# Kernel tuning notes

Hardware: AMD Instinct MI355X
Metric: run time of the kernel (lower is better)

The kernel has to match this reference:

```python
import jax, jax.numpy as jnp
import numpy as np

N_HEAD = 8
TOTAL_DIM = 64   # trans dim: num_node*f_dim + arV_dim = 15*4 + 4
F_DIM = 4        # node_feature_dim
NUM_NODE = 15
EPS = 1e-5


def _ln(x, g, b):
    m = jnp.mean(x, axis=-1, keepdims=True)
    v = jnp.var(x, axis=-1, keepdims=True)
    return (x - m) * jax.lax.rsqrt(v + EPS) * g + b


def setup_inputs() -> dict:
    key = jax.random.key(0)
    B, T, C, L, V = 4, 1024, 1024, 4, 100
    ks = jax.random.split(key, 16)
    g = lambda k, sh, s=0.02: jax.random.normal(k, sh, jnp.float32) * s
    return {
        'x': jax.random.normal(ks[0], (B, T, C), jnp.float32),
        'attn_bias': jax.random.normal(ks[1], (N_HEAD, NUM_NODE, NUM_NODE), jnp.float32),
        'pos_emb': g(ks[2], (1, T, C)),
        'Wq': g(ks[3], (L, C, C)), 'bq': jnp.zeros((L, C), jnp.float32),
        'Wk': g(ks[4], (L, C, C)), 'bk': jnp.zeros((L, C), jnp.float32),
        'Wv': g(ks[5], (L, C, C)), 'bv': jnp.zeros((L, C), jnp.float32),
        'Wp': g(ks[6], (L, C, C)), 'bp': jnp.zeros((L, C), jnp.float32),
        'ln1_g': jnp.ones((L, C), jnp.float32), 'ln1_b': jnp.zeros((L, C), jnp.float32),
        'ln2_g': jnp.ones((L, C), jnp.float32), 'ln2_b': jnp.zeros((L, C), jnp.float32),
        'w1': g(ks[7], (L, C, 4 * C)), 'b1': jnp.zeros((L, 4 * C), jnp.float32),
        'w2': g(ks[8], (L, 4 * C, C)), 'b2': jnp.zeros((L, C), jnp.float32),
        'lnf_g': jnp.ones((C,), jnp.float32), 'lnf_b': jnp.zeros((C,), jnp.float32),
        'head_w': g(ks[9], (TOTAL_DIM, V + 1, C)),
    }


def reference(x, attn_bias, pos_emb, Wq, bq, Wk, bk, Wv, bv, Wp, bp,
              ln1_g, ln1_b, ln2_g, ln2_b, w1, b1, w2, b2, lnf_g, lnf_b, head_w):
    B, T, C = x.shape
    L = Wq.shape[0]
    hd = C // N_HEAD
    scale = 1.0 / np.sqrt(hd).astype(np.float32)

    # expand graph bias: bias[h, i*f+a, j*f+b] = attn_bias[h, i, j]
    d = NUM_NODE * F_DIM
    bias = jnp.repeat(jnp.repeat(attn_bias, F_DIM, axis=1), F_DIM, axis=2)  # [nh, d, d]
    pbias = jnp.zeros((N_HEAD, T, T), x.dtype).at[:, :d, :d].set(bias)      # [nh, T, T]

    # causal mask with every TOTAL_DIM-th column disabled
    mask = jnp.tril(jnp.ones((T, T), bool))
    mask = mask & ((jnp.arange(T) % TOTAL_DIM) != TOTAL_DIM - 1)[None, :]

    h = x + pos_emb[:, :T]
    neg_inf = jnp.asarray(-jnp.inf, x.dtype)
    for l in range(L):  # fixed small layer count
        a = _ln(h, ln1_g[l], ln1_b[l])
        q = (a @ Wq[l] + bq[l]).reshape(B, T, N_HEAD, hd).transpose(0, 2, 1, 3)
        k = (a @ Wk[l] + bk[l]).reshape(B, T, N_HEAD, hd).transpose(0, 2, 1, 3)
        v = (a @ Wv[l] + bv[l]).reshape(B, T, N_HEAD, hd).transpose(0, 2, 1, 3)
        att = jnp.einsum('bhid,bhjd->bhij', q, k) * scale + pbias[None]
        att = jnp.where(mask[None, None], att, neg_inf)
        att = jax.nn.softmax(att, axis=-1)
        y = jnp.einsum('bhij,bhjd->bhid', att, v).transpose(0, 2, 1, 3).reshape(B, T, C)
        h = h + y @ Wp[l] + bp[l]
        a2 = _ln(h, ln2_g[l], ln2_b[l])
        h = h + jax.nn.gelu(a2 @ w1[l] + b1[l], approximate=False) @ w2[l] + b2[l]

    h = _ln(h, lnf_g, lnf_b)
    # pad_to_full_observation + EinLinear head
    n_pad = (-T) % TOTAL_DIM
    hp = jnp.pad(h, ((0, 0), (0, n_pad), (0, 0))).reshape(-1, TOTAL_DIM, C)
    logits = jnp.einsum('eoi,bei->beo', head_w, hp)
    return logits.reshape(B, T + n_pad, -1)[:, :T]
```

## Files before the change

### kernel.cpp

```cpp
#include <hip/hip_runtime.h>
#include <cstdint>

#define DEV __device__ __forceinline__

typedef unsigned short u16;
typedef __attribute__((ext_vector_type(8))) short bf16x8;
typedef __attribute__((ext_vector_type(4))) unsigned short u16x4;
typedef __attribute__((ext_vector_type(4))) float f32x4;

typedef __attribute__((address_space(1))) const void GV;
typedef __attribute__((address_space(3))) void LV;

DEV float b2f(u16 u) { uint32_t i = ((uint32_t)u) << 16; return __builtin_bit_cast(float, i); }
DEV u16 f2b(float f) {
    uint32_t i = __builtin_bit_cast(uint32_t, f);
    return (u16)((i + 0x7fffu + ((i >> 16) & 1u)) >> 16);
}
DEV void load_lds16(const void* g, void* l) {
    __builtin_amdgcn_global_load_lds((GV*)g, (LV*)l, 16, 0, 0);
}

__global__ __launch_bounds__(256) void k_addpos(const float* __restrict__ x,
                                                const float* __restrict__ pos,
                                                float* __restrict__ h) {
    size_t i = (size_t)blockIdx.x * 256 + threadIdx.x;
    f32x4 a = *(const f32x4*)(x + i * 4);
    f32x4 p = *(const f32x4*)(pos + ((i * 4) & 1048575));
    a += p;
    *(f32x4*)(h + i * 4) = a;
}

__global__ __launch_bounds__(256) void k_transcvt(const float* __restrict__ W,
                                                  u16* __restrict__ WT, int K, int N,
                                                  size_t ozs) {
    __shared__ float t[32][33];
    size_t zin = (size_t)blockIdx.z * K * N, zout = (size_t)blockIdx.z * ozs;
    int n0 = blockIdx.x * 32, k0 = blockIdx.y * 32;
    int r = threadIdx.x >> 3, c = (threadIdx.x & 7) << 2;
    f32x4 v = *(const f32x4*)(W + zin + (size_t)(k0 + r) * N + n0 + c);
    t[r][c] = v[0]; t[r][c + 1] = v[1]; t[r][c + 2] = v[2]; t[r][c + 3] = v[3];
    __syncthreads();
    u16x4 o;
    o[0] = f2b(t[c][r]); o[1] = f2b(t[c + 1][r]); o[2] = f2b(t[c + 2][r]); o[3] = f2b(t[c + 3][r]);
    *(u16x4*)(WT + zout + (size_t)(n0 + r) * K + k0 + c) = o;
}

__global__ __launch_bounds__(256) void k_cvt(const float* __restrict__ in,
                                             u16* __restrict__ out, int n4) {
    int i = blockIdx.x * 256 + threadIdx.x;
    if (i < n4) {
        f32x4 v = *(const f32x4*)(in + (size_t)i * 4);
        u16x4 o; o[0] = f2b(v[0]); o[1] = f2b(v[1]); o[2] = f2b(v[2]); o[3] = f2b(v[3]);
        *(u16x4*)(out + (size_t)i * 4) = o;
    }
}

__global__ __launch_bounds__(256) void k_packb(const float* __restrict__ bq,
                                               const float* __restrict__ bk,
                                               const float* __restrict__ bv,
                                               float* __restrict__ bqkv) {
    int l = blockIdx.x;
    for (int i = threadIdx.x; i < 1024; i += 256) {
        bqkv[l * 3072 + i]        = bq[l * 1024 + i];
        bqkv[l * 3072 + 1024 + i] = bk[l * 1024 + i];
        bqkv[l * 3072 + 2048 + i] = bv[l * 1024 + i];
    }
}

__global__ __launch_bounds__(256) void k_ln(const float* __restrict__ in,
                                            const float* __restrict__ g,
                                            const float* __restrict__ bta,
                                            u16* __restrict__ out) {
    int row = blockIdx.x, tid = threadIdx.x;
    const float* rp = in + (size_t)row * 1024;
    f32x4 v = *(const f32x4*)(rp + tid * 4);
    float s = v[0] + v[1] + v[2] + v[3];
    float ss = v[0] * v[0] + v[1] * v[1] + v[2] * v[2] + v[3] * v[3];
    #pragma unroll
    for (int off = 32; off; off >>= 1) { s += __shfl_down(s, off); ss += __shfl_down(ss, off); }
    __shared__ float rs[4], rss[4];
    int wave = tid >> 6, lane = tid & 63;
    if (!lane) { rs[wave] = s; rss[wave] = ss; }
    __syncthreads();
    float ts = rs[0] + rs[1] + rs[2] + rs[3];
    float tss = rss[0] + rss[1] + rss[2] + rss[3];
    float mean = ts * (1.0f / 1024.0f);
    float var = tss * (1.0f / 1024.0f) - mean * mean;
    float rstd = rsqrtf(var + 1e-5f);
    f32x4 gv = *(const f32x4*)(g + tid * 4);
    f32x4 bv = *(const f32x4*)(bta + tid * 4);
    u16x4 o;
    #pragma unroll
    for (int j = 0; j < 4; ++j) o[j] = f2b((v[j] - mean) * rstd * gv[j] + bv[j]);
    *(u16x4*)(out + (size_t)row * 1024 + tid * 4) = o;
}

__global__ __launch_bounds__(256) void k_gemmr(const u16* __restrict__ A,
                                               const u16* __restrict__ BT,
                                               const float* __restrict__ bias,
                                               float* __restrict__ H,
                                               int M, int N, int K) {
    __shared__ __align__(16) u16 As[2][64 * 64];
    __shared__ __align__(16) u16 Bs[2][128 * 64];
    const int tid = threadIdx.x, lane = tid & 63, wave = tid >> 6;
    const int wy = wave >> 1, wx = wave & 1;
    const int lcol = lane & 15, lrow = lane >> 4;

    const int nbx = gridDim.x, nwg = nbx * gridDim.y;
    int id = blockIdx.y * nbx + blockIdx.x;
    int q = nwg >> 3, r = nwg & 7;
    int xcd = id & 7, pos = id >> 3;
    int nid = (xcd < r ? xcd * (q + 1) : r * (q + 1) + (xcd - r) * q) + pos;
    const int m0 = (nid / nbx) * 64, n0 = (nid % nbx) * 128;
    const int NT = K >> 6;

    f32x4 acc[2][4] = {};

    auto stage = [&](int buf, int kt) {
        int k0 = kt << 6;
        #pragma unroll
        for (int it = 0; it < 2; ++it) {
            int c = it * 256 + tid;
            int row = c >> 3, s = (c & 7) ^ (row & 7);
            load_lds16(A + (size_t)(m0 + row) * K + k0 + s * 8,
                       &As[buf][(it * 256 + wave * 64) * 8]);
        }
        #pragma unroll
        for (int it = 0; it < 4; ++it) {
            int c = it * 256 + tid;
            int row = c >> 3, s = (c & 7) ^ (row & 7);
            load_lds16(BT + (size_t)(n0 + row) * K + k0 + s * 8,
                       &Bs[buf][(it * 256 + wave * 64) * 8]);
        }
    };

    stage(0, 0);
    for (int kt = 0; kt < NT; ++kt) {
        __syncthreads();
        if (kt + 1 < NT) stage((kt + 1) & 1, kt + 1);
        const u16* ab = As[kt & 1];
        const u16* bb = Bs[kt & 1];
        #pragma unroll
        for (int kc = 0; kc < 2; ++kc) {
            bf16x8 af[2], bfr[4];
            #pragma unroll
            for (int mi = 0; mi < 2; ++mi) {
                int mrow = wy * 32 + mi * 16 + lcol;
                int s = (kc * 4 + lrow) ^ (mrow & 7);
                af[mi] = *(const bf16x8*)(ab + mrow * 64 + s * 8);
            }
            #pragma unroll
            for (int ni = 0; ni < 4; ++ni) {
                int nrow = wx * 64 + ni * 16 + lcol;
                int s = (kc * 4 + lrow) ^ (nrow & 7);
                bfr[ni] = *(const bf16x8*)(bb + nrow * 64 + s * 8);
            }
            #pragma unroll
            for (int mi = 0; mi < 2; ++mi)
                #pragma unroll
                for (int ni = 0; ni < 4; ++ni)
                    acc[mi][ni] = __builtin_amdgcn_mfma_f32_16x16x32_bf16(af[mi], bfr[ni], acc[mi][ni], 0, 0, 0);
        }
    }

    #pragma unroll
    for (int mi = 0; mi < 2; ++mi) {
        #pragma unroll
        for (int ni = 0; ni < 4; ++ni) {
            int col = n0 + wx * 64 + ni * 16 + lcol;
            float bcol = bias[col];
            #pragma unroll
            for (int r2 = 0; r2 < 4; ++r2) {
                int row = m0 + wy * 32 + mi * 16 + lrow * 4 + r2;
                float* o = H + (size_t)row * N + col;
                *o = *o + acc[mi][ni][r2] + bcol;
            }
        }
    }
}

template <int EPI>
__global__ __launch_bounds__(512) void k_g128(const u16* __restrict__ A,
                                              const u16* __restrict__ BT,
                                              const float* __restrict__ bias,
                                              u16* __restrict__ Cout,
                                              int M, int N, int K) {
    __shared__ __align__(16) u16 As[2][4096];
    __shared__ __align__(16) u16 Bs[2][8192];
    const int tid = threadIdx.x, lane = tid & 63, wave = tid >> 6;
    const int wy = wave >> 2, wx = wave & 3;
    const int lcol = lane & 15, lrow = lane >> 4;

    const int nbx = gridDim.x, nwg = nbx * gridDim.y;
    int id = blockIdx.y * nbx + blockIdx.x;
    int q = nwg >> 3, r = nwg & 7;
    int xcd = id & 7, pos = id >> 3;
    int nid = (xcd < r ? xcd * (q + 1) : r * (q + 1) + (xcd - r) * q) + pos;
    const int m0 = (nid / nbx) * 128, n0 = (nid % nbx) * 256;
    const int NT = K >> 5;

    f32x4 acc[4][4] = {};

    auto stage = [&](int buf, int kt) {
        int k0 = kt << 5;
        {
            int c = tid;
            int row = c >> 2, s = (c & 3) ^ ((row >> 1) & 3);
            load_lds16(A + (size_t)(m0 + row) * K + k0 + s * 8,
                       &As[buf][(wave * 64) * 8]);
        }
        #pragma unroll
        for (int it = 0; it < 2; ++it) {
            int c = it * 512 + tid;
            int row = c >> 2, s = (c & 3) ^ ((row >> 1) & 3);
            load_lds16(BT + (size_t)(n0 + row) * K + k0 + s * 8,
                       &Bs[buf][(it * 512 + wave * 64) * 8]);
        }
    };

    stage(0, 0);
    for (int kt = 0; kt < NT; ++kt) {
        __syncthreads();
        if (kt + 1 < NT) stage((kt + 1) & 1, kt + 1);
        const u16* ab = As[kt & 1];
        const u16* bb = Bs[kt & 1];
        bf16x8 bfr[4];
        #pragma unroll
        for (int ni = 0; ni < 4; ++ni) {
            int nrow = wx * 64 + ni * 16 + lcol;
            bfr[ni] = *(const bf16x8*)(bb + nrow * 32 + ((lrow ^ ((nrow >> 1) & 3)) * 8));
        }
        #pragma unroll
        for (int mi = 0; mi < 4; ++mi) {
            int mrow = wy * 64 + mi * 16 + lcol;
            bf16x8 af = *(const bf16x8*)(ab + mrow * 32 + ((lrow ^ ((mrow >> 1) & 3)) * 8));
            #pragma unroll
            for (int ni = 0; ni < 4; ++ni)
                acc[mi][ni] = __builtin_amdgcn_mfma_f32_16x16x32_bf16(af, bfr[ni], acc[mi][ni], 0, 0, 0);
        }
    }

    #pragma unroll
    for (int mi = 0; mi < 4; ++mi) {
        #pragma unroll
        for (int ni = 0; ni < 4; ++ni) {
            int col = n0 + wx * 64 + ni * 16 + lcol;
            float bcol = bias[col];
            #pragma unroll
            for (int r2 = 0; r2 < 4; ++r2) {
                int row = m0 + wy * 64 + mi * 16 + lrow * 4 + r2;
                float val = acc[mi][ni][r2] + bcol;
                if constexpr (EPI == 1)
                    val = 0.5f * val * (1.0f + erff(val * 0.70710678118654752f));
                Cout[(size_t)row * N + col] = f2b(val);
            }
        }
    }
}

__global__ __launch_bounds__(256) void k_attn(const u16* __restrict__ qkv,
                                              const float* __restrict__ abias,
                                              u16* __restrict__ yb) {
    __shared__ __align__(16) u16 Ks[2][64 * 128];
    __shared__ __align__(16) u16 Vt[2][128 * 64];
    __shared__ __align__(16) u16 Ps[4][16 * 72];

    const int idx = blockIdx.x;
    const int half = idx >> 8, u = idx & 255;
    const int qt = half ? (15 - (u & 15)) : (u & 15);
    const int h = (u >> 4) & 7;
    const int b = (u >> 7) + half * 2;

    const int tid = threadIdx.x, wave = tid >> 6, lane = tid & 63;
    const int lcol = lane & 15, lrow = lane >> 4;
    const int q0 = qt * 64 + wave * 16;
    const size_t base = (size_t)b * 1024 * 3072 + h * 128;
    const u16* qp = qkv + base;
    const u16* kp = qkv + base + 1024;
    const u16* vp = qkv + base + 2048;
    u16* psw = Ps[wave];
    const int j4 = tid & 15, d8 = tid >> 4;

    bf16x8 aq[4];
    #pragma unroll
    for (int df = 0; df < 4; ++df)
        aq[df] = *(const bf16x8*)(qp + (size_t)(q0 + lcol) * 3072 + df * 32 + lrow * 8);

    f32x4 o[8];
    #pragma unroll
    for (int i = 0; i < 8; ++i) o[i] = f32x4{0.f, 0.f, 0.f, 0.f};
    float mrun[4], lrun[4];
    #pragma unroll
    for (int r = 0; r < 4; ++r) { mrun[r] = -__builtin_inff(); lrun[r] = 0.f; }

    const float scale = 0.08838834764831845f;
    const int nt = qt + 1;

    auto k_issue = [&](int buf, int t) {
        const int j0 = t * 64;
        #pragma unroll
        for (int it = 0; it < 4; ++it) {
            int c = it * 256 + wave * 64 + lane;
            int row = c >> 4, slot = c & 15;
            int sslot = slot ^ (row & 7);
            load_lds16(kp + (size_t)(j0 + row) * 3072 + sslot * 8,
                       &Ks[buf][(it * 256 + wave * 64) * 8]);
        }
    };
    auto v_issue = [&](int t, bf16x8* vr) {
        const int j0 = t * 64;
        #pragma unroll
        for (int r = 0; r < 4; ++r)
            vr[r] = *(const bf16x8*)(vp + (size_t)(j0 + j4 * 4 + r) * 3072 + d8 * 8);
    };
    auto v_write = [&](int buf, const bf16x8* vr) {
        #pragma unroll
        for (int i = 0; i < 8; ++i) {
            int d = d8 * 8 + i;
            u16x4 w;
            w[0] = (u16)vr[0][i]; w[1] = (u16)vr[1][i]; w[2] = (u16)vr[2][i]; w[3] = (u16)vr[3][i];
            *(u16x4*)(&Vt[buf][d * 64 + ((j4 * 4) ^ (i << 3))]) = w;
        }
    };

    bf16x8 v0r[4];
    k_issue(0, 0);
    v_issue(0, v0r);
    v_write(0, v0r);

    for (int t = 0; t < nt; ++t) {
        __syncthreads();
        const int cur = t & 1, nxt = cur ^ 1;
        const bool more = (t + 1 < nt);
        bf16x8 vn[4];
        if (more) { k_issue(nxt, t + 1); v_issue(t + 1, vn); }

        const u16* ks = Ks[cur];
        const u16* vt = Vt[cur];
        const int j0 = t * 64;

        f32x4 S[4];
        #pragma unroll
        for (int sub = 0; sub < 4; ++sub) {
            const int row = sub * 16 + lcol;
            const int sw = row & 7;
            f32x4 s = {};
            #pragma unroll
            for (int df = 0; df < 4; ++df) {
                bf16x8 kf = *(const bf16x8*)(ks + row * 128 + ((df * 4 + lrow) ^ sw) * 8);
                s = __builtin_amdgcn_mfma_f32_16x16x32_bf16(aq[df], kf, s, 0, 0, 0);
            }
            S[sub] = s;
        }

        float p[4][4], tmax[4];
        #pragma unroll
        for (int r = 0; r < 4; ++r) tmax[r] = -__builtin_inff();
        #pragma unroll
        for (int sub = 0; sub < 4; ++sub) {
            const int kj = j0 + sub * 16 + lcol;
            #pragma unroll
            for (int r = 0; r < 4; ++r) {
                const int qi = q0 + lrow * 4 + r;
                float v = S[sub][r] * scale;
                if (qi < 60 && kj < 60) v += abias[(h * 15 + (qi >> 2)) * 15 + (kj >> 2)];
                v = ((kj <= qi) && ((kj & 63) != 63)) ? v : -__builtin_inff();
                p[sub][r] = v;
                tmax[r] = fmaxf(tmax[r], v);
            }
        }
        #pragma unroll
        for (int off = 1; off < 16; off <<= 1)
            #pragma unroll
            for (int r = 0; r < 4; ++r) tmax[r] = fmaxf(tmax[r], __shfl_xor(tmax[r], off));
        float alpha[4], rsum[4];
        #pragma unroll
        for (int r = 0; r < 4; ++r) {
            float mnew = fmaxf(mrun[r], tmax[r]);
            alpha[r] = __expf(mrun[r] - mnew);
            mrun[r] = mnew;
            float acc = 0.f;
            #pragma unroll
            for (int sub = 0; sub < 4; ++sub) { p[sub][r] = __expf(p[sub][r] - mnew); acc += p[sub][r]; }
            rsum[r] = acc;
        }
        #pragma unroll
        for (int off = 1; off < 16; off <<= 1)
            #pragma unroll
            for (int r = 0; r < 4; ++r) rsum[r] += __shfl_xor(rsum[r], off);
        #pragma unroll
        for (int r = 0; r < 4; ++r) lrun[r] = lrun[r] * alpha[r] + rsum[r];
        #pragma unroll
        for (int i = 0; i < 8; ++i)
            #pragma unroll
            for (int r = 0; r < 4; ++r) o[i][r] *= alpha[r];

        #pragma unroll
        for (int sub = 0; sub < 4; ++sub)
            #pragma unroll
            for (int r = 0; r < 4; ++r)
                psw[(lrow * 4 + r) * 72 + sub * 16 + lcol] = f2b(p[sub][r]);

        #pragma unroll
        for (int kt = 0; kt < 2; ++kt) {
            bf16x8 pa = *(const bf16x8*)(psw + lcol * 72 + kt * 32 + lrow * 8);
            #pragma unroll
            for (int of = 0; of < 8; ++of) {
                const int d = of * 16 + lcol;
                bf16x8 vf = *(const bf16x8*)(vt + d * 64 + ((kt * 32 + lrow * 8) ^ ((d & 7) << 3)));
                o[of] = __builtin_amdgcn_mfma_f32_16x16x32_bf16(pa, vf, o[of], 0, 0, 0);
            }
        }

        if (more) v_write(nxt, vn);
    }

    u16* yp = yb + (size_t)b * 1024 * 1024 + h * 128;
    #pragma unroll
    for (int of = 0; of < 8; ++of)
        #pragma unroll
        for (int r = 0; r < 4; ++r) {
            int row = q0 + lrow * 4 + r;
            yp[(size_t)row * 1024 + of * 16 + lcol] = f2b(o[of][r] / lrun[r]);
        }
}

__global__ __launch_bounds__(256) void k_head(const u16* __restrict__ hln,
                                              const u16* __restrict__ hw16,
                                              float* __restrict__ out) {
    const int e = blockIdx.x, bq = blockIdx.y;
    const int lane = threadIdx.x & 63, wave = threadIdx.x >> 6;
    const int lcol = lane & 15, lrow = lane >> 4;

    const u16* ap = hln + ((size_t)bq * 1024 + lcol * 64 + e) * 1024 + lrow * 8;
    const int nt0 = wave, nt1 = wave + 4;
    const int oo0 = nt0 * 16 + lcol, oo1 = nt1 * 16 + lcol;
    const bool v0 = oo0 < 101;
    const bool has1 = nt1 < 7;
    const bool v1 = has1 && (oo1 < 101);
    const u16* bp0 = hw16 + ((size_t)e * 101 + (v0 ? oo0 : 0)) * 1024 + lrow * 8;
    const u16* bp1 = hw16 + ((size_t)e * 101 + (v1 ? oo1 : 0)) * 1024 + lrow * 8;

    f32x4 acc0 = {}, acc1 = {};
    #pragma unroll 4
    for (int kt = 0; kt < 32; ++kt) {
        bf16x8 af = *(const bf16x8*)(ap + kt * 32);
        bf16x8 b0 = {};
        if (v0) b0 = *(const bf16x8*)(bp0 + kt * 32);
        acc0 = __builtin_amdgcn_mfma_f32_16x16x32_bf16(af, b0, acc0, 0, 0, 0);
        if (has1) {
            bf16x8 b1 = {};
            if (v1) b1 = *(const bf16x8*)(bp1 + kt * 32);
            acc1 = __builtin_amdgcn_mfma_f32_16x16x32_bf16(af, b1, acc1, 0, 0, 0);
        }
    }

    #pragma unroll
    for (int r = 0; r < 4; ++r) {
        size_t row = (size_t)bq * 1024 + (lrow * 4 + r) * 64 + e;
        if (v0) out[row * 101 + oo0] = acc0[r];
        if (v1) out[row * 101 + oo1] = acc1[r];
    }
}

extern "C" void kernel_launch(void* const* d_in, const int* in_sizes, int n_in,
                              void* d_out, int out_size, void* d_ws, size_t ws_size,
                              hipStream_t stream) {
    (void)in_sizes; (void)n_in; (void)out_size; (void)ws_size;
    const float* x     = (const float*)d_in[0];
    const float* abias = (const float*)d_in[1];
    const float* pos   = (const float*)d_in[2];
    const float* Wq    = (const float*)d_in[3];
    const float* bq    = (const float*)d_in[4];
    const float* Wk    = (const float*)d_in[5];
    const float* bk    = (const float*)d_in[6];
    const float* Wv    = (const float*)d_in[7];
    const float* bv    = (const float*)d_in[8];
    const float* Wp    = (const float*)d_in[9];
    const float* bp    = (const float*)d_in[10];
    const float* ln1g  = (const float*)d_in[11];
    const float* ln1b  = (const float*)d_in[12];
    const float* ln2g  = (const float*)d_in[13];
    const float* ln2b  = (const float*)d_in[14];
    const float* w1    = (const float*)d_in[15];
    const float* b1    = (const float*)d_in[16];
    const float* w2    = (const float*)d_in[17];
    const float* b2    = (const float*)d_in[18];
    const float* lnfg  = (const float*)d_in[19];
    const float* lnfb  = (const float*)d_in[20];
    const float* hw    = (const float*)d_in[21];
    float* out = (float*)d_out;

    char* ws = (char*)d_ws;
    size_t off = 0;
    auto alloc = [&](size_t bytes) { void* p = ws + off; off += (bytes + 255) & ~(size_t)255; return p; };
    float* H    = (float*)alloc(4096ull * 1024 * 4);
    u16* ABF    = (u16*)alloc(4096ull * 1024 * 2);
    char* R     = (char*)alloc(4096ull * 4096 * 2);
    u16* QKV    = (u16*)R;
    u16* YB     = (u16*)(R + 4096ull * 3072 * 2);
    u16* MB     = (u16*)R;
    u16* WQKV   = (u16*)alloc(4ull * 3072 * 1024 * 2);
    u16* WPT    = (u16*)alloc(4ull * 1024 * 1024 * 2);
    u16* W1T    = (u16*)alloc(4ull * 1024 * 4096 * 2);
    u16* W2T    = (u16*)alloc(4ull * 4096 * 1024 * 2);
    u16* HW16   = (u16*)alloc(64ull * 101 * 1024 * 2);
    float* BQKV = (float*)alloc(4ull * 3072 * 4);

    dim3 blk(256);
    const size_t QS = 3072ull * 1024;
    k_transcvt<<<dim3(32, 32, 4), blk, 0, stream>>>(Wq, WQKV,                    1024, 1024, QS);
    k_transcvt<<<dim3(32, 32, 4), blk, 0, stream>>>(Wk, WQKV + 1024ull * 1024,   1024, 1024, QS);
    k_transcvt<<<dim3(32, 32, 4), blk, 0, stream>>>(Wv, WQKV + 2048ull * 1024,   1024, 1024, QS);
    k_transcvt<<<dim3(32, 32, 4), blk, 0, stream>>>(Wp, WPT, 1024, 1024, 1048576);
    k_transcvt<<<dim3(128, 32, 4), blk, 0, stream>>>(w1, W1T, 1024, 4096, 4194304);
    k_transcvt<<<dim3(32, 128, 4), blk, 0, stream>>>(w2, W2T, 4096, 1024, 4194304);
    k_cvt<<<dim3(64 * 101 * 1024 / 4 / 256), blk, 0, stream>>>(hw, HW16, 64 * 101 * 1024 / 4);
    k_packb<<<dim3(4), blk, 0, stream>>>(bq, bk, bv, BQKV);
    k_addpos<<<dim3(4096), blk, 0, stream>>>(x, pos, H);

    for (int l = 0; l < 4; ++l) {
        k_ln<<<dim3(4096), blk, 0, stream>>>(H, ln1g + l * 1024, ln1b + l * 1024, ABF);
        k_g128<0><<<dim3(12, 32), dim3(512), 0, stream>>>(ABF, WQKV + (size_t)l * QS, BQKV + l * 3072, QKV, 4096, 3072, 1024);
        k_attn<<<dim3(512), blk, 0, stream>>>(QKV, abias, YB);
        k_gemmr<<<dim3(8, 64), blk, 0, stream>>>(YB, WPT + (size_t)l * 1048576, bp + l * 1024, H, 4096, 1024, 1024);
        k_ln<<<dim3(4096), blk, 0, stream>>>(H, ln2g + l * 1024, ln2b + l * 1024, ABF);
        k_g128<1><<<dim3(16, 32), dim3(512), 0, stream>>>(ABF, W1T + (size_t)l * 4194304, b1 + l * 4096, MB, 4096, 4096, 1024);
        k_gemmr<<<dim3(8, 64), blk, 0, stream>>>(MB, W2T + (size_t)l * 4194304, b2 + l * 1024, H, 4096, 1024, 4096);
    }
    k_ln<<<dim3(4096), blk, 0, stream>>>(H, lnfg, lnfb, ABF);
    k_head<<<dim3(64, 4), blk, 0, stream>>>(ABF, HW16, out);
}
```

Before: 1.035 ms.

## Triple-buffer residual GEMM LDS pipeline with explicit waitcnt and setprio

Changes the k_gemmr residual GEMM from double to triple LDS buffering, prefetching two K-tiles ahead. It replaces __syncthreads with raw s_barrier plus explicit vmcnt waits, so global-to-LDS loads can stay in flight across iterations. All LDS fragments are loaded before the MFMA block, which is wrapped in s_setprio to favour the matrix work. LDS use grows to 72KB per block, which may reduce occupancy. The hand-placed waitcnts also carry a correctness risk.

```diff
diff --git a/kernel.cpp b/kernel.cpp
--- a/kernel.cpp
+++ b/kernel.cpp
@@ -100,8 +100,8 @@
                                                const float* __restrict__ bias,
                                                float* __restrict__ H,
                                                int M, int N, int K) {
-    __shared__ __align__(16) u16 As[2][64 * 64];
-    __shared__ __align__(16) u16 Bs[2][128 * 64];
+    __shared__ __align__(16) u16 As[3][64 * 64];
+    __shared__ __align__(16) u16 Bs[3][128 * 64];
     const int tid = threadIdx.x, lane = tid & 63, wave = tid >> 6;
     const int wy = wave >> 1, wx = wave & 1;
     const int lcol = lane & 15, lrow = lane >> 4;
@@ -116,51 +116,69 @@
 
     f32x4 acc[2][4] = {};
 
-    auto stage = [&](int buf, int kt) {
+    auto stage = [&](int bi, int kt) {
         int k0 = kt << 6;
         #pragma unroll
         for (int it = 0; it < 2; ++it) {
             int c = it * 256 + tid;
             int row = c >> 3, s = (c & 7) ^ (row & 7);
             load_lds16(A + (size_t)(m0 + row) * K + k0 + s * 8,
-                       &As[buf][(it * 256 + wave * 64) * 8]);
+                       &As[bi][(it * 256 + wave * 64) * 8]);
         }
         #pragma unroll
         for (int it = 0; it < 4; ++it) {
             int c = it * 256 + tid;
             int row = c >> 3, s = (c & 7) ^ (row & 7);
             load_lds16(BT + (size_t)(n0 + row) * K + k0 + s * 8,
-                       &Bs[buf][(it * 256 + wave * 64) * 8]);
+                       &Bs[bi][(it * 256 + wave * 64) * 8]);
         }
     };
 
     stage(0, 0);
+    if (NT > 1) stage(1, 1);
+    asm volatile("s_waitcnt vmcnt(6)" ::: "memory");
+    __builtin_amdgcn_sched_barrier(0);
+
+    int cur = 0;
     for (int kt = 0; kt < NT; ++kt) {
-        __syncthreads();
-        if (kt + 1 < NT) stage((kt + 1) & 1, kt + 1);
-        const u16* ab = As[kt & 1];
-        const u16* bb = Bs[kt & 1];
+        __builtin_amdgcn_s_barrier();
+        if (kt + 2 < NT) {
+            int nb = cur + 2; if (nb >= 3) nb -= 3;
+            stage(nb, kt + 2);
+        }
+        const u16* ab = As[cur];
+        const u16* bb = Bs[cur];
+        bf16x8 af[2][2], bfr[2][4];
         #pragma unroll
         for (int kc = 0; kc < 2; ++kc) {
-            bf16x8 af[2], bfr[4];
             #pragma unroll
             for (int mi = 0; mi < 2; ++mi) {
                 int mrow = wy * 32 + mi * 16 + lcol;
                 int s = (kc * 4 + lrow) ^ (mrow & 7);
-                af[mi] = *(const bf16x8*)(ab + mrow * 64 + s * 8);
+                af[kc][mi] = *(const bf16x8*)(ab + mrow * 64 + s * 8);
             }
             #pragma unroll
             for (int ni = 0; ni < 4; ++ni) {
                 int nrow = wx * 64 + ni * 16 + lcol;
                 int s = (kc * 4 + lrow) ^ (nrow & 7);
-                bfr[ni] = *(const bf16x8*)(bb + nrow * 64 + s * 8);
-            }
+                bfr[kc][ni] = *(const bf16x8*)(bb + nrow * 64 + s * 8);
+            }
+        }
+        asm volatile("s_waitcnt lgkmcnt(0)" ::: "memory");
+        __builtin_amdgcn_sched_barrier(0);
+        __builtin_amdgcn_s_setprio(1);
+        #pragma unroll
+        for (int kc = 0; kc < 2; ++kc)
             #pragma unroll
             for (int mi = 0; mi < 2; ++mi)
                 #pragma unroll
                 for (int ni = 0; ni < 4; ++ni)
-                    acc[mi][ni] = __builtin_amdgcn_mfma_f32_16x16x32_bf16(af[mi], bfr[ni], acc[mi][ni], 0, 0, 0);
-        }
+                    acc[mi][ni] = __builtin_amdgcn_mfma_f32_16x16x32_bf16(af[kc][mi], bfr[kc][ni], acc[mi][ni], 0, 0, 0);
+        __builtin_amdgcn_s_setprio(0);
+        if (kt + 2 < NT) { asm volatile("s_waitcnt vmcnt(6)" ::: "memory"); }
+        else             { asm volatile("s_waitcnt vmcnt(0)" ::: "memory"); }
+        __builtin_amdgcn_sched_barrier(0);
+        cur = cur + 1; if (cur >= 3) cur -= 3;
     }
 
     #pragma unroll
```

After: 1.052 ms. No clear change (+1.6%).
